# Optimization experiments

Measured on AMD Instinct MI355X. Metric: run time of the kernel, lower is better.

## Reference

```python
import jax, jax.numpy as jnp
import numpy as np

OUTDIM, INPUTDIM, DEGREE = 64, 512, 8


def setup_inputs() -> dict:
    key = jax.random.key(0)
    k1, k2 = jax.random.split(key)
    x = jax.random.normal(k1, (16, 4096, INPUTDIM), dtype=jnp.float32)
    # torch.randn(outdim, inputdim, degree) / (sqrt(inputdim)*sqrt(degree))
    coeffs = jax.random.normal(k2, (OUTDIM, INPUTDIM, DEGREE), dtype=jnp.float32)
    coeffs = coeffs / (np.sqrt(INPUTDIM) * np.sqrt(DEGREE))
    bias = jnp.zeros((1, OUTDIM), dtype=jnp.float32)
    return {"x": x, "coeffs": coeffs, "bias": bias}


def _legendre_basis(xn, degree):
    # Iterative (memoized) Legendre recurrence; xn in [-1, 1], shape [N, I].
    Ps = [jnp.ones_like(xn)]
    if degree > 1:
        Ps.append(xn)
    for n in range(2, degree):
        Ps.append(((2.0 * n - 1.0) * xn * Ps[-1] - (n - 1.0) * Ps[-2]) / n)
    return jnp.stack(Ps, axis=-1)  # [N, I, D]


def reference(x, coeffs, bias):
    outdim, inputdim, degree = coeffs.shape
    outshape = x.shape[:-1] + (outdim,)
    x2 = x.reshape(-1, inputdim)                      # [N, I]
    xmin, xmax = x2.min(), x2.max()                   # global min-max normalize
    xn = 2.0 * (x2 - xmin) / (xmax - xmin) - 1.0
    P = _legendre_basis(xn, degree)                   # [N, I, D]
    y = jnp.einsum("nid,oid->no", P, coeffs)          # contract input & degree
    y = y + bias                                      # [N, O]
    return y.reshape(outshape)
```

## Files before the change

kernel.cpp:

```cpp
#include <hip/hip_runtime.h>
#include <math.h>


typedef __bf16 bf16x8 __attribute__((ext_vector_type(8)));
typedef float f32x4 __attribute__((ext_vector_type(4)));

__global__ __launch_bounds__(256) void k_minmax_partial(
    const float4* __restrict__ x4, int n4, float* __restrict__ pmn, float* __restrict__ pmx)
{
  float mn = 3.4e38f, mx = -3.4e38f;
  int stride = gridDim.x * 256;
  for (int i = blockIdx.x * 256 + threadIdx.x; i < n4; i += stride) {
    float4 v = x4[i];
    mn = fminf(mn, fminf(fminf(v.x, v.y), fminf(v.z, v.w)));
    mx = fmaxf(mx, fmaxf(fmaxf(v.x, v.y), fmaxf(v.z, v.w)));
  }
  #pragma unroll
  for (int off = 32; off > 0; off >>= 1) {
    mn = fminf(mn, __shfl_down(mn, off));
    mx = fmaxf(mx, __shfl_down(mx, off));
  }
  __shared__ float smn[4], smx[4];
  int w = threadIdx.x >> 6;
  if ((threadIdx.x & 63) == 0) { smn[w] = mn; smx[w] = mx; }
  __syncthreads();
  if (threadIdx.x == 0) {
    pmn[blockIdx.x] = fminf(fminf(smn[0], smn[1]), fminf(smn[2], smn[3]));
    pmx[blockIdx.x] = fmaxf(fmaxf(smx[0], smx[1]), fmaxf(smx[2], smx[3]));
  }
}

__global__ __launch_bounds__(256) void k_prep_final(
    const float* __restrict__ coeffs, bf16x8* __restrict__ Bws,
    const float* __restrict__ pmn, const float* __restrict__ pmx, int nb,
    float* __restrict__ so)
{
  if (blockIdx.x < 128) {
    int t = blockIdx.x * 256 + threadIdx.x;
    int lane = t & 63;
    int tile = t >> 6;
    int ct = tile & 3;
    int kt = tile >> 2;
    int i = kt * 4 + (lane >> 4);
    int o = ct * 16 + (lane & 15);
    const float4* cp = (const float4*)(coeffs + ((size_t)o * 512 + i) * 8);
    float4 c0 = cp[0], c1 = cp[1];
    bf16x8 v;
    v[0] = (__bf16)(c0.x);
    v[1] = (__bf16)(c0.y);
    v[2] = (__bf16)(c0.z * 1.5f);
    v[3] = (__bf16)(c0.w * 2.5f);
    v[4] = (__bf16)(c1.x * 4.375f);
    v[5] = (__bf16)(c1.y * 7.875f);
    v[6] = (__bf16)(c1.z * 14.4375f);
    v[7] = (__bf16)(c1.w * 26.8125f);
    Bws[(size_t)(kt * 4 + ct) * 64 + lane] = v;
  } else {
    float mn = 3.4e38f, mx = -3.4e38f;
    for (int i = threadIdx.x; i < nb; i += 256) {
      mn = fminf(mn, pmn[i]);
      mx = fmaxf(mx, pmx[i]);
    }
    #pragma unroll
    for (int off = 32; off > 0; off >>= 1) {
      mn = fminf(mn, __shfl_down(mn, off));
      mx = fmaxf(mx, __shfl_down(mx, off));
    }
    __shared__ float smn[4], smx[4];
    int w = threadIdx.x >> 6;
    if ((threadIdx.x & 63) == 0) { smn[w] = mn; smx[w] = mx; }
    __syncthreads();
    if (threadIdx.x == 0) {
      mn = fminf(fminf(smn[0], smn[1]), fminf(smn[2], smn[3]));
      mx = fmaxf(fmaxf(smx[0], smx[1]), fmaxf(smx[2], smx[3]));
      float r = mx - mn;
      so[0] = 2.0f / r;
      so[1] = -2.0f * mn / r - 1.0f;
    }
  }
}

#define LSTW 20
__global__ __launch_bounds__(256, 3) void k_main(
    const float* __restrict__ x, const bf16x8* __restrict__ Bws,
    const float* __restrict__ bias, const float* __restrict__ so,
    float* __restrict__ y)
{
  __shared__ char smem[49152];

  const float s = so[0], off = so[1];
  const int t    = threadIdx.x;
  const int lane = t & 63;
  const int w    = t >> 6;
  const int m    = lane & 15;
  const int quad = lane >> 4;
  const size_t blockRow = (size_t)blockIdx.x * 64;

  float* xsw = (float*)(smem + w * (2 * 64 * LSTW * 4));
  const float* xg = x + (blockRow + lane) * 512 + w * 128;

  int rb[4];
  #pragma unroll
  for (int f = 0; f < 4; ++f) rb[f] = (f * 16 + m) * LSTW + quad;

  const bf16x8* Bp = Bws + (size_t)w * 32 * 256 + lane;

  f32x4 acc[4][4];
  #pragma unroll
  for (int f = 0; f < 4; ++f)
    #pragma unroll
    for (int ct = 0; ct < 4; ++ct) acc[f][ct] = (f32x4){0.f, 0.f, 0.f, 0.f};

  const float C2 = 0.33333334f, C3 = 0.26666668f, C4 = 0.25714287f;
  const float C5 = 0.25396827f, C6 = 0.25252524f, C7 = 0.25174826f;

  float4 st[4];
  #pragma unroll
  for (int p = 0; p < 4; ++p) st[p] = *(const float4*)(xg + p * 4);
  #pragma unroll
  for (int p = 0; p < 4; ++p) *(float4*)&xsw[lane * LSTW + p * 4] = st[p];

  bf16x8 Bq[4][4];
  #pragma unroll
  for (int ct = 0; ct < 4; ++ct) {
    Bq[0][ct] = Bp[ct * 64];
    Bq[1][ct] = Bp[256 + ct * 64];
  }

  for (int c = 0; c < 8; ++c) {
    float* xr = xsw + (c & 1) * (64 * LSTW);

    if (c < 7) {
      const float* gp = xg + (c + 1) * 16;
      #pragma unroll
      for (int p = 0; p < 4; ++p) st[p] = *(const float4*)(gp + p * 4);
    }

    float xv[2][4];
    #pragma unroll
    for (int f = 0; f < 4; ++f) xv[0][f] = xr[rb[f]];

    #pragma unroll
    for (int ktl = 0; ktl < 4; ++ktl) {
      const int l = c * 4 + ktl;

      {
        const int kp = (l + 2) & 31;
        const bf16x8* bpk = Bp + (size_t)kp * 256;
        #pragma unroll
        for (int ct = 0; ct < 4; ++ct) Bq[(ktl + 2) & 3][ct] = bpk[ct * 64];
      }
      if (ktl < 3) {
        #pragma unroll
        for (int f = 0; f < 4; ++f)
          xv[(ktl + 1) & 1][f] = xr[rb[f] + (ktl + 1) * 4];
      }

      bf16x8 a[4];
      #pragma unroll
      for (int f = 0; f < 4; ++f) {
        float xn = fmaf(xv[ktl & 1][f], s, off);
        float s2 = fmaf(xn, xn, -C2);
        float s3 = (s2 - C3) * xn;
        float s4 = fmaf(xn, s3, -(C4 * s2));
        float s5 = fmaf(xn, s4, -(C5 * s3));
        float s6 = fmaf(xn, s5, -(C6 * s4));
        float s7 = fmaf(xn, s6, -(C7 * s5));
        bf16x8 av;
        av[0] = (__bf16)1.0f; av[1] = (__bf16)xn; av[2] = (__bf16)s2; av[3] = (__bf16)s3;
        av[4] = (__bf16)s4;   av[5] = (__bf16)s5; av[6] = (__bf16)s6; av[7] = (__bf16)s7;
        a[f] = av;
      }

      #pragma unroll
      for (int f = 0; f < 4; ++f)
        #pragma unroll
        for (int ct = 0; ct < 4; ++ct)
          acc[f][ct] = __builtin_amdgcn_mfma_f32_16x16x32_bf16(a[f], Bq[ktl & 3][ct], acc[f][ct], 0, 0, 0);
    }

    if (c < 7) {
      float* xw = xsw + ((c + 1) & 1) * (64 * LSTW);
      #pragma unroll
      for (int p = 0; p < 4; ++p) *(float4*)&xw[lane * LSTW + p * 4] = st[p];
    }
  }

  __syncthreads();
  f32x4* red = (f32x4*)smem;
  if (w > 0) {
    #pragma unroll
    for (int f = 0; f < 4; ++f)
      #pragma unroll
      for (int ct = 0; ct < 4; ++ct)
        red[(size_t)(w - 1) * 1024 + (f * 4 + ct) * 64 + lane] = acc[f][ct];
  }
  __syncthreads();
  if (w == 0) {
    #pragma unroll
    for (int f = 0; f < 4; ++f)
      #pragma unroll
      for (int ct = 0; ct < 4; ++ct) {
        f32x4 v = acc[f][ct];
        v += red[(f * 4 + ct) * 64 + lane];
        v += red[1024 + (f * 4 + ct) * 64 + lane];
        v += red[2048 + (f * 4 + ct) * 64 + lane];
        acc[f][ct] = v;
      }
    float bv0 = bias[m], bv1 = bias[16 + m], bv2 = bias[32 + m], bv3 = bias[48 + m];
    #pragma unroll
    for (int f = 0; f < 4; ++f) {
      float* yp = y + (blockRow + f * 16 + quad * 4) * 64 + m;
      #pragma unroll
      for (int r = 0; r < 4; ++r) {
        float* ypr = yp + r * 64;
        ypr[0]  = acc[f][0][r] + bv0;
        ypr[16] = acc[f][1][r] + bv1;
        ypr[32] = acc[f][2][r] + bv2;
        ypr[48] = acc[f][3][r] + bv3;
      }
    }
  }
}

__global__ __launch_bounds__(256) void k_main_simple(
    const float* __restrict__ x, const float* __restrict__ coeffs,
    const float* __restrict__ bias, const float* __restrict__ so, float* __restrict__ y)
{
  const float s = so[0], off = so[1];
  const int lane = threadIdx.x & 63;
  const int w    = threadIdx.x >> 6;
  const int m    = lane & 15;
  const int quad = lane >> 4;
  const int rowA = blockIdx.x * 64 + w * 16 + m;
  const float* xp = x + (size_t)rowA * 512 + quad;

  f32x4 acc0 = {0.f,0.f,0.f,0.f}, acc1 = acc0, acc2 = acc0, acc3 = acc0;
  const float c3a = 5.f/3.f, c3b = 2.f/3.f, c6a = 11.f/6.f, c6b = 5.f/6.f, c7a = 13.f/7.f, c7b = 6.f/7.f;

  for (int kt = 0; kt < 128; ++kt) {
    float xv = xp[kt * 4];
    int i = kt * 4 + quad;
    bf16x8 b[4];
    #pragma unroll
    for (int ct = 0; ct < 4; ++ct) {
      const float* cp = coeffs + ((size_t)(ct * 16 + m) * 512 + i) * 8;
      #pragma unroll
      for (int j = 0; j < 8; ++j) b[ct][j] = (__bf16)cp[j];
    }
    float xn = fmaf(xv, s, off);
    float p2 = fmaf(1.5f * xn, xn, -0.5f);
    float p3 = fmaf(c3a * xn, p2, -(c3b * xn));
    float p4 = fmaf(1.75f * xn, p3, -(0.75f * p2));
    float p5 = fmaf(1.8f * xn, p4, -(0.8f * p3));
    float p6 = fmaf(c6a * xn, p5, -(c6b * p4));
    float p7 = fmaf(c7a * xn, p6, -(c7b * p5));
    bf16x8 a;
    a[0] = (__bf16)1.0f; a[1] = (__bf16)xn; a[2] = (__bf16)p2; a[3] = (__bf16)p3;
    a[4] = (__bf16)p4;   a[5] = (__bf16)p5; a[6] = (__bf16)p6; a[7] = (__bf16)p7;
    acc0 = __builtin_amdgcn_mfma_f32_16x16x32_bf16(a, b[0], acc0, 0, 0, 0);
    acc1 = __builtin_amdgcn_mfma_f32_16x16x32_bf16(a, b[1], acc1, 0, 0, 0);
    acc2 = __builtin_amdgcn_mfma_f32_16x16x32_bf16(a, b[2], acc2, 0, 0, 0);
    acc3 = __builtin_amdgcn_mfma_f32_16x16x32_bf16(a, b[3], acc3, 0, 0, 0);
  }
  float b0v = bias[m], b1v = bias[16+m], b2v = bias[32+m], b3v = bias[48+m];
  float* yp = y + ((size_t)(blockIdx.x * 64 + w * 16 + quad * 4)) * 64 + m;
  #pragma unroll
  for (int r = 0; r < 4; ++r) {
    yp[r*64+ 0] = acc0[r] + b0v;
    yp[r*64+16] = acc1[r] + b1v;
    yp[r*64+32] = acc2[r] + b2v;
    yp[r*64+48] = acc3[r] + b3v;
  }
}

extern "C" void kernel_launch(void* const* d_in, const int* in_sizes, int n_in,
                              void* d_out, int out_size, void* d_ws, size_t ws_size,
                              hipStream_t stream)
{
  const float* x      = (const float*)d_in[0];
  const float* coeffs = (const float*)d_in[1];
  const float* bias   = (const float*)d_in[2];
  float* y = (float*)d_out;

  long nx = (long)in_sizes[0];
  int  N  = (int)(nx / 512);
  int  n4 = (int)(nx / 4);

  float*  so  = (float*)d_ws;
  float*  pmn = (float*)d_ws + 16;
  float*  pmx = pmn + 4096;
  bf16x8* Bws = (bf16x8*)((char*)d_ws + 65536);

  const int MMB = 2048;
  k_minmax_partial<<<MMB, 256, 0, stream>>>((const float4*)x, n4, pmn, pmx);

  bool pre = ws_size >= (size_t)(65536 + 4096 * 64 * 2 + 4096);
  k_prep_final<<<129, 256, 0, stream>>>(coeffs, Bws, pmn, pmx, MMB, so);
  if (pre) {
    k_main<<<N / 64, 256, 0, stream>>>(x, Bws, bias, so, y);
  } else {
    k_main_simple<<<N / 64, 256, 0, stream>>>(x, coeffs, bias, so, y);
  }
}
```

Before: 251.7 us.

## Merge prep kernels, fold final min-max into main, stage x via global_load_lds

Merges the coefficient repacking into the min-max partial kernel and drops the separate finalize kernel. Each main-kernel block now reduces the 2048 partials itself, removing one launch and one serialization point. The main kernel stages x tiles into LDS with direct global-to-LDS loads, using an XOR-swizzled layout instead of register round-trips. It adds a block-wide barrier per chunk and redundant partial reductions in every block.

```diff
diff --git a/kernel.cpp b/kernel.cpp
--- a/kernel.cpp
+++ b/kernel.cpp
@@ -5,45 +5,26 @@
 typedef __bf16 bf16x8 __attribute__((ext_vector_type(8)));
 typedef float f32x4 __attribute__((ext_vector_type(4)));
 
-__global__ __launch_bounds__(256) void k_minmax_partial(
-    const float4* __restrict__ x4, int n4, float* __restrict__ pmn, float* __restrict__ pmx)
-{
-  float mn = 3.4e38f, mx = -3.4e38f;
-  int stride = gridDim.x * 256;
-  for (int i = blockIdx.x * 256 + threadIdx.x; i < n4; i += stride) {
-    float4 v = x4[i];
-    mn = fminf(mn, fminf(fminf(v.x, v.y), fminf(v.z, v.w)));
-    mx = fmaxf(mx, fmaxf(fmaxf(v.x, v.y), fmaxf(v.z, v.w)));
-  }
-  #pragma unroll
-  for (int off = 32; off > 0; off >>= 1) {
-    mn = fminf(mn, __shfl_down(mn, off));
-    mx = fmaxf(mx, __shfl_down(mx, off));
-  }
-  __shared__ float smn[4], smx[4];
-  int w = threadIdx.x >> 6;
-  if ((threadIdx.x & 63) == 0) { smn[w] = mn; smx[w] = mx; }
-  __syncthreads();
-  if (threadIdx.x == 0) {
-    pmn[blockIdx.x] = fminf(fminf(smn[0], smn[1]), fminf(smn[2], smn[3]));
-    pmx[blockIdx.x] = fmaxf(fmaxf(smx[0], smx[1]), fmaxf(smx[2], smx[3]));
-  }
-}
-
-__global__ __launch_bounds__(256) void k_prep_final(
-    const float* __restrict__ coeffs, bf16x8* __restrict__ Bws,
-    const float* __restrict__ pmn, const float* __restrict__ pmx, int nb,
-    float* __restrict__ so)
-{
-  if (blockIdx.x < 128) {
+__device__ __forceinline__ void gload_lds16(const float* g, void* lds) {
+  __builtin_amdgcn_global_load_lds(
+      static_cast<const unsigned int*>(static_cast<const void*>(g)),
+      static_cast<unsigned int*>(lds), 16, 0, 0);
+}
+
+__global__ __launch_bounds__(256) void k_pre(
+    const float4* __restrict__ x4, int n4,
+    float* __restrict__ pmn, float* __restrict__ pmx,
+    const float* __restrict__ coeffs, bf16x8* __restrict__ Bws, int doprep)
+{
+  if (doprep && blockIdx.x < 128) {
     int t = blockIdx.x * 256 + threadIdx.x;
     int lane = t & 63;
     int tile = t >> 6;
     int ct = tile & 3;
     int kt = tile >> 2;
-    int i = kt * 4 + (lane >> 4);
-    int o = ct * 16 + (lane & 15);
-    const float4* cp = (const float4*)(coeffs + ((size_t)o * 512 + i) * 8);
+    int ii = kt * 4 + (lane >> 4);
+    int o  = ct * 16 + (lane & 15);
+    const float4* cp = (const float4*)(coeffs + ((size_t)o * 512 + ii) * 8);
     float4 c0 = cp[0], c1 = cp[1];
     bf16x8 v;
     v[0] = (__bf16)(c0.x);
@@ -55,40 +36,37 @@
     v[6] = (__bf16)(c1.z * 14.4375f);
     v[7] = (__bf16)(c1.w * 26.8125f);
     Bws[(size_t)(kt * 4 + ct) * 64 + lane] = v;
-  } else {
-    float mn = 3.4e38f, mx = -3.4e38f;
-    for (int i = threadIdx.x; i < nb; i += 256) {
-      mn = fminf(mn, pmn[i]);
-      mx = fmaxf(mx, pmx[i]);
-    }
-    #pragma unroll
-    for (int off = 32; off > 0; off >>= 1) {
-      mn = fminf(mn, __shfl_down(mn, off));
-      mx = fmaxf(mx, __shfl_down(mx, off));
-    }
-    __shared__ float smn[4], smx[4];
-    int w = threadIdx.x >> 6;
-    if ((threadIdx.x & 63) == 0) { smn[w] = mn; smx[w] = mx; }
-    __syncthreads();
-    if (threadIdx.x == 0) {
-      mn = fminf(fminf(smn[0], smn[1]), fminf(smn[2], smn[3]));
-      mx = fmaxf(fmaxf(smx[0], smx[1]), fmaxf(smx[2], smx[3]));
-      float r = mx - mn;
-      so[0] = 2.0f / r;
-      so[1] = -2.0f * mn / r - 1.0f;
-    }
-  }
-}
-
-#define LSTW 20
+  }
+  float mn = 3.4e38f, mx = -3.4e38f;
+  int stride = gridDim.x * 256;
+  for (int i = blockIdx.x * 256 + threadIdx.x; i < n4; i += stride) {
+    float4 v = x4[i];
+    mn = fminf(mn, fminf(fminf(v.x, v.y), fminf(v.z, v.w)));
+    mx = fmaxf(mx, fmaxf(fmaxf(v.x, v.y), fmaxf(v.z, v.w)));
+  }
+  #pragma unroll
+  for (int off = 32; off > 0; off >>= 1) {
+    mn = fminf(mn, __shfl_down(mn, off));
+    mx = fmaxf(mx, __shfl_down(mx, off));
+  }
+  __shared__ float smn[4], smx[4];
+  int w = threadIdx.x >> 6;
+  if ((threadIdx.x & 63) == 0) { smn[w] = mn; smx[w] = mx; }
+  __syncthreads();
+  if (threadIdx.x == 0) {
+    pmn[blockIdx.x] = fminf(fminf(smn[0], smn[1]), fminf(smn[2], smn[3]));
+    pmx[blockIdx.x] = fmaxf(fmaxf(smx[0], smx[1]), fmaxf(smx[2], smx[3]));
+  }
+}
+
+#define NPART 2048
 __global__ __launch_bounds__(256, 3) void k_main(
     const float* __restrict__ x, const bf16x8* __restrict__ Bws,
-    const float* __restrict__ bias, const float* __restrict__ so,
-    float* __restrict__ y)
-{
-  __shared__ char smem[49152];
-
-  const float s = so[0], off = so[1];
+    const float* __restrict__ bias, const float* __restrict__ pmn,
+    const float* __restrict__ pmx, float* __restrict__ y)
+{
+  __shared__ __attribute__((aligned(16))) char smem[49152];
+
   const int t    = threadIdx.x;
   const int lane = t & 63;
   const int w    = t >> 6;
@@ -96,70 +74,90 @@
   const int quad = lane >> 4;
   const size_t blockRow = (size_t)blockIdx.x * 64;
 
-  float* xsw = (float*)(smem + w * (2 * 64 * LSTW * 4));
-  const float* xg = x + (blockRow + lane) * 512 + w * 128;
-
-  int rb[4];
-  #pragma unroll
-  for (int f = 0; f < 4; ++f) rb[f] = (f * 16 + m) * LSTW + quad;
-
-  const bf16x8* Bp = Bws + (size_t)w * 32 * 256 + lane;
+  const float* gp[4];
+  #pragma unroll
+  for (int p = 0; p < 4; ++p) {
+    int r15 = 4 * p + quad;
+    int row = 16 * w + r15;
+    int cfl = m ^ r15;
+    gp[p] = x + (size_t)(blockRow + row) * 512 + cfl * 4;
+  }
+  #pragma unroll
+  for (int p = 0; p < 4; ++p)
+    gload_lds16(gp[p], smem + (w * 4 + p) * 1024);
+
+  float mn = 3.4e38f, mx = -3.4e38f;
+  #pragma unroll
+  for (int j = 0; j < NPART / 64; ++j) {
+    mn = fminf(mn, pmn[lane + j * 64]);
+    mx = fmaxf(mx, pmx[lane + j * 64]);
+  }
+  #pragma unroll
+  for (int o2 = 32; o2 > 0; o2 >>= 1) {
+    mn = fminf(mn, __shfl_xor(mn, o2));
+    mx = fmaxf(mx, __shfl_xor(mx, o2));
+  }
+  const float s   = 2.0f / (mx - mn);
+  const float off = fmaf(-mn, s, -1.0f);
+
+  bf16x8 Bq[4][4];
+  #pragma unroll
+  for (int ct = 0; ct < 4; ++ct) {
+    Bq[0][ct] = Bws[(size_t)((4 * w + 0) * 4 + ct) * 64 + lane];
+    Bq[1][ct] = Bws[(size_t)((4 * w + 1) * 4 + ct) * 64 + lane];
+  }
 
   f32x4 acc[4][4];
   #pragma unroll
   for (int f = 0; f < 4; ++f)
     #pragma unroll
     for (int ct = 0; ct < 4; ++ct) acc[f][ct] = (f32x4){0.f, 0.f, 0.f, 0.f};
+
+  int xbase[4], xo[4];
+  #pragma unroll
+  for (int f = 0; f < 4; ++f) xbase[f] = (f * 16 + m) * 64 + quad;
+  #pragma unroll
+  for (int k = 0; k < 4; ++k) xo[k] = ((4 * w + k) ^ m) << 2;
 
   const float C2 = 0.33333334f, C3 = 0.26666668f, C4 = 0.25714287f;
   const float C5 = 0.25396827f, C6 = 0.25252524f, C7 = 0.25174826f;
 
-  float4 st[4];
-  #pragma unroll
-  for (int p = 0; p < 4; ++p) st[p] = *(const float4*)(xg + p * 4);
-  #pragma unroll
-  for (int p = 0; p < 4; ++p) *(float4*)&xsw[lane * LSTW + p * 4] = st[p];
-
-  bf16x8 Bq[4][4];
-  #pragma unroll
-  for (int ct = 0; ct < 4; ++ct) {
-    Bq[0][ct] = Bp[ct * 64];
-    Bq[1][ct] = Bp[256 + ct * 64];
-  }
+  __syncthreads();
 
   for (int c = 0; c < 8; ++c) {
-    float* xr = xsw + (c & 1) * (64 * LSTW);
+    const float* xr = (const float*)(smem + (c & 1) * 16384);
 
     if (c < 7) {
-      const float* gp = xg + (c + 1) * 16;
-      #pragma unroll
-      for (int p = 0; p < 4; ++p) st[p] = *(const float4*)(gp + p * 4);
+      char* lb = smem + ((c + 1) & 1) * 16384;
+      #pragma unroll
+      for (int p = 0; p < 4; ++p)
+        gload_lds16(gp[p] + (c + 1) * 64, lb + (w * 4 + p) * 1024);
     }
 
-    float xv[2][4];
-    #pragma unroll
-    for (int f = 0; f < 4; ++f) xv[0][f] = xr[rb[f]];
+    float xvv[2][4];
+    #pragma unroll
+    for (int f = 0; f < 4; ++f) xvv[0][f] = xr[xbase[f] + xo[0]];
 
     #pragma unroll
     for (int ktl = 0; ktl < 4; ++ktl) {
       const int l = c * 4 + ktl;
 
       {
-        const int kp = (l + 2) & 31;
-        const bf16x8* bpk = Bp + (size_t)kp * 256;
+        const int lp  = (l + 2) & 31;
+        const int ktg = ((lp >> 2) << 4) + 4 * w + (lp & 3);
         #pragma unroll
-        for (int ct = 0; ct < 4; ++ct) Bq[(ktl + 2) & 3][ct] = bpk[ct * 64];
+        for (int ct = 0; ct < 4; ++ct)
+          Bq[(ktl + 2) & 3][ct] = Bws[(size_t)(ktg * 4 + ct) * 64 + lane];
       }
       if (ktl < 3) {
         #pragma unroll
         for (int f = 0; f < 4; ++f)
-          xv[(ktl + 1) & 1][f] = xr[rb[f] + (ktl + 1) * 4];
-      }
-
-      bf16x8 a[4];
+          xvv[(ktl + 1) & 1][f] = xr[xbase[f] + xo[ktl + 1]];
+      }
+
       #pragma unroll
       for (int f = 0; f < 4; ++f) {
-        float xn = fmaf(xv[ktl & 1][f], s, off);
+        float xn = fmaf(xvv[ktl & 1][f], s, off);
         float s2 = fmaf(xn, xn, -C2);
         float s3 = (s2 - C3) * xn;
         float s4 = fmaf(xn, s3, -(C4 * s2));
@@ -169,24 +167,14 @@
         bf16x8 av;
         av[0] = (__bf16)1.0f; av[1] = (__bf16)xn; av[2] = (__bf16)s2; av[3] = (__bf16)s3;
         av[4] = (__bf16)s4;   av[5] = (__bf16)s5; av[6] = (__bf16)s6; av[7] = (__bf16)s7;
-        a[f] = av;
-      }
-
-      #pragma unroll
-      for (int f = 0; f < 4; ++f)
         #pragma unroll
         for (int ct = 0; ct < 4; ++ct)
-          acc[f][ct] = __builtin_amdgcn_mfma_f32_16x16x32_bf16(a[f], Bq[ktl & 3][ct], acc[f][ct], 0, 0, 0);
+          acc[f][ct] = __builtin_amdgcn_mfma_f32_16x16x32_bf16(av, Bq[ktl & 3][ct], acc[f][ct], 0, 0, 0);
+      }
     }
-
-    if (c < 7) {
-      float* xw = xsw + ((c + 1) & 1) * (64 * LSTW);
-      #pragma unroll
-      for (int p = 0; p < 4; ++p) *(float4*)&xw[lane * LSTW + p * 4] = st[p];
-    }
-  }
-
-  __syncthreads();
+    __syncthreads();
+  }
+
   f32x4* red = (f32x4*)smem;
   if (w > 0) {
     #pragma unroll
@@ -220,6 +208,33 @@
         ypr[48] = acc[f][3][r] + bv3;
       }
     }
+  }
+}
+
+__global__ __launch_bounds__(256) void k_so(
+    const float* __restrict__ pmn, const float* __restrict__ pmx, int nb,
+    float* __restrict__ so)
+{
+  float mn = 3.4e38f, mx = -3.4e38f;
+  for (int i = threadIdx.x; i < nb; i += 256) {
+    mn = fminf(mn, pmn[i]);
+    mx = fmaxf(mx, pmx[i]);
+  }
+  #pragma unroll
+  for (int off = 32; off > 0; off >>= 1) {
+    mn = fminf(mn, __shfl_down(mn, off));
+    mx = fmaxf(mx, __shfl_down(mx, off));
+  }
+  __shared__ float smn[4], smx[4];
+  int w = threadIdx.x >> 6;
+  if ((threadIdx.x & 63) == 0) { smn[w] = mn; smx[w] = mx; }
+  __syncthreads();
+  if (threadIdx.x == 0) {
+    mn = fminf(fminf(smn[0], smn[1]), fminf(smn[2], smn[3]));
+    mx = fmaxf(fmaxf(smx[0], smx[1]), fmaxf(smx[2], smx[3]));
+    float r = mx - mn;
+    so[0] = 2.0f / r;
+    so[1] = -2.0f * mn / r - 1.0f;
   }
 }
 
@@ -292,14 +307,12 @@
   float*  pmx = pmn + 4096;
   bf16x8* Bws = (bf16x8*)((char*)d_ws + 65536);
 
-  const int MMB = 2048;
-  k_minmax_partial<<<MMB, 256, 0, stream>>>((const float4*)x, n4, pmn, pmx);
-
   bool pre = ws_size >= (size_t)(65536 + 4096 * 64 * 2 + 4096);
-  k_prep_final<<<129, 256, 0, stream>>>(coeffs, Bws, pmn, pmx, MMB, so);
+  k_pre<<<NPART, 256, 0, stream>>>((const float4*)x, n4, pmn, pmx, coeffs, Bws, pre ? 1 : 0);
   if (pre) {
-    k_main<<<N / 64, 256, 0, stream>>>(x, Bws, bias, so, y);
+    k_main<<<N / 64, 256, 0, stream>>>(x, Bws, bias, pmn, pmx, y);
   } else {
+    k_so<<<1, 256, 0, stream>>>(pmn, pmx, NPART, so);
     k_main_simple<<<N / 64, 256, 0, stream>>>(x, coeffs, bias, so, y);
   }
 }
```

After: 242.0 us. 3.9% less time.
